# Optimization experiments

Measured on AMD Instinct MI355X. Metric: run time of the kernel, lower is better.

## Reference

```python
import jax, jax.numpy as jnp
import numpy as np

B, L, V = 128, 32, 10000
IC, WD, H = 2048, 512, 512  # image_code_dim, word_dim, hidden_size (num_layers=1)
D = WD + IC  # GRU input dim


def setup_inputs() -> dict:
    key = jax.random.key(0)
    ks = jax.random.split(key, 10)
    image_code = jax.random.normal(ks[0], (B, IC), dtype=jnp.float32)
    captions = jax.random.randint(ks[1], (B, L), 0, V)
    cap_lens = jax.random.randint(ks[2], (B,), 2, L + 1)
    cap_lens = cap_lens.at[0].set(L)  # pin max length -> static T = L-1
    # parameters (embed/fc match init_weights uniform(-0.1,0.1); GRU/init_state ~ small random)
    embed_w = jax.random.uniform(ks[3], (V, WD), minval=-0.1, maxval=0.1, dtype=jnp.float32)
    W_ih = jax.random.normal(ks[4], (3 * H, D), dtype=jnp.float32) * 0.02
    W_hh = jax.random.normal(ks[5], (3 * H, H), dtype=jnp.float32) * 0.02
    b_ih = jnp.zeros((3 * H,), dtype=jnp.float32)
    b_hh = jnp.zeros((3 * H,), dtype=jnp.float32)
    fc_w = jax.random.uniform(ks[6], (V, H), minval=-0.1, maxval=0.1, dtype=jnp.float32)
    fc_b = jnp.zeros((V,), dtype=jnp.float32)
    init_w = jax.random.normal(ks[7], (H, IC), dtype=jnp.float32) * 0.02  # num_layers*H x IC
    init_b = jnp.zeros((H,), dtype=jnp.float32)
    return {"image_code": image_code, "captions": captions, "cap_lens": cap_lens,
            "embed_w": embed_w, "W_ih": W_ih, "W_hh": W_hh, "b_ih": b_ih, "b_hh": b_hh,
            "fc_w": fc_w, "fc_b": fc_b, "init_w": init_w, "init_b": init_b}


def _gru_decode(image_code, captions_s, lengths, h0, embed_w, W_ih, W_hh, b_ih, b_hh, fc_w, fc_b):
    T = L - 1
    emb = embed_w[captions_s]                      # (B, L, WD)
    xs = jnp.concatenate([
        jnp.broadcast_to(image_code[None], (T, B, IC)),
        jnp.transpose(emb[:, :T, :], (1, 0, 2)),   # (T, B, WD)
    ], axis=-1)                                    # (T, B, D)

    def step(h, x_t):
        gi = x_t @ W_ih.T + b_ih                   # (B, 3H)
        gh = h @ W_hh.T + b_hh                     # (B, 3H)
        i_r, i_z, i_n = jnp.split(gi, 3, axis=-1)
        h_r, h_z, h_n = jnp.split(gh, 3, axis=-1)
        r = jax.nn.sigmoid(i_r + h_r)
        z = jax.nn.sigmoid(i_z + h_z)
        n = jnp.tanh(i_n + r * h_n)
        h_new = (1.0 - z) * n + z * h
        return h_new, h_new

    _, outs = jax.lax.scan(step, h0, xs)           # (T, B, H)
    preds = jnp.einsum('tbh,vh->tbv', outs, fc_w) + fc_b  # dropout is identity in eval
    mask = jnp.arange(T)[:, None] < lengths[None, :]      # (T, B): only active steps
    preds = jnp.where(mask[:, :, None], preds, 0.0)
    return jnp.transpose(preds, (1, 0, 2))         # (B, T, V)


def reference(image_code, captions, cap_lens, embed_w, W_ih, W_hh, b_ih, b_hh, fc_w, fc_b, init_w, init_b):
    order = jnp.argsort(-cap_lens)                 # descending sort like torch.sort(..., True)
    sorted_lens = cap_lens[order]
    captions_s = captions[order]
    image_code_s = image_code[order]
    h0 = image_code_s @ init_w.T + init_b          # (B, H) (num_layers = 1)
    lengths = sorted_lens - 1
    predictions = _gru_decode(image_code_s, captions_s, lengths, h0,
                              embed_w, W_ih, W_hh, b_ih, b_hh, fc_w, fc_b)
    return predictions, captions_s, lengths, order
```

## Files before the change

### kernel.cpp

```cpp
#include <hip/hip_runtime.h>
#include <math.h>

#define B_   128
#define L_   32
#define T_   31
#define V_   10000
#define IC_  2048
#define WD_  512
#define H_   512
#define D_   2560
#define G3_  1536
#define NPAD_ 10112
#define NPROD_ 64
#define NCONS_ 395
#define NTEAM_ 5

typedef short short8 __attribute__((ext_vector_type(8)));
typedef float f32x4  __attribute__((ext_vector_type(4)));
typedef unsigned short ushort_t;
typedef unsigned long long ull_t;

__device__ __forceinline__ unsigned short f2bf(float f) {
    unsigned int u = __builtin_bit_cast(unsigned int, f);
    unsigned int r = (u + 0x7FFFu + ((u >> 16) & 1u)) >> 16;
    return (unsigned short)r;
}
__device__ __forceinline__ float bf2f(unsigned short h) {
    unsigned int u = ((unsigned int)h) << 16;
    return __builtin_bit_cast(float, u);
}
__device__ __forceinline__ f32x4 mfma16(short8 a, short8 b, f32x4 c) {
    return __builtin_amdgcn_mfma_f32_16x16x32_bf16(a, b, c, 0, 0, 0);
}

#define WS_ORDER  0
#define WS_LEN    512
#define WS_TOK    1024
#define WS_BAR    16896
#define WS_GIIMG  16960
#define WS_WHH    803392
#define WS_GIFULL 2376256
#define WS_OUTS   14565952
#define WS_FCW    18760256

__global__ void k_prep(const int* __restrict__ captions,
                       const int* __restrict__ cap_lens,
                       int* __restrict__ order,
                       int* __restrict__ len_i,
                       int* __restrict__ tok,
                       int* __restrict__ bar,
                       float* __restrict__ out_tail) {
    __shared__ int s_len[B_];
    __shared__ int s_ord[B_];
    const int tid = threadIdx.x;
    if (tid == 0) *bar = 0;
    if (tid < B_) s_len[tid] = cap_lens[tid];
    __syncthreads();
    if (tid < B_) {
        const int myl = s_len[tid];
        int rank = 0;
        for (int k = 0; k < B_; ++k) {
            const int lk = s_len[k];
            if (lk > myl || (lk == myl && k < tid)) rank++;
        }
        s_ord[rank] = tid;
    }
    __syncthreads();
    if (tid < B_) {
        const int o = s_ord[tid];
        order[tid] = o;
        const int ln = s_len[o] - 1;
        len_i[tid] = ln;
        out_tail[B_ * L_ + tid]      = (float)ln;
        out_tail[B_ * L_ + B_ + tid] = (float)o;
    }
    __syncthreads();
    for (int i = tid; i < B_ * L_; i += blockDim.x) {
        const int b = i / L_, l = i % L_;
        const int c = captions[s_ord[b] * L_ + l];
        out_tail[i] = (float)c;
        if (l < T_) tok[l * B_ + b] = c;
    }
}

__global__ void k_cvt_fcw(const float* __restrict__ src, ushort_t* __restrict__ dst) {
    const int idx = blockIdx.x * 256 + threadIdx.x;
    const int row = idx >> 6;
    const int ch  = idx & 63;
    union { unsigned short u[8]; uint4 v; } r;
    if (row < V_) {
        const float* p = src + (size_t)row * 512 + ch * 8;
        const float4 x = *(const float4*)p;
        const float4 y = *(const float4*)(p + 4);
        r.u[0]=f2bf(x.x); r.u[1]=f2bf(x.y); r.u[2]=f2bf(x.z); r.u[3]=f2bf(x.w);
        r.u[4]=f2bf(y.x); r.u[5]=f2bf(y.y); r.u[6]=f2bf(y.z); r.u[7]=f2bf(y.w);
    } else {
        r.v = make_uint4(0, 0, 0, 0);
    }
    *(uint4*)&dst[(size_t)row * 512 + ch * 8] = r.v;
}

__global__ void k_cvt_whh(const float* __restrict__ whh, ushort_t* __restrict__ dst) {
    const int idx = blockIdx.x * 256 + threadIdx.x;
    const size_t o = (size_t)idx * 8;
    const int g = (int)(o / (48 * 512));
    const int rem = (int)(o % (48 * 512));
    const int j = rem >> 9;
    const int k = rem & 511;
    const int srow = (j >> 4) * 512 + g * 16 + (j & 15);
    const float* p = whh + (size_t)srow * 512 + k;
    const float4 x = *(const float4*)p;
    const float4 y = *(const float4*)(p + 4);
    union { unsigned short u[8]; uint4 v; } r;
    r.u[0]=f2bf(x.x); r.u[1]=f2bf(x.y); r.u[2]=f2bf(x.z); r.u[3]=f2bf(x.w);
    r.u[4]=f2bf(y.x); r.u[5]=f2bf(y.y); r.u[6]=f2bf(y.z); r.u[7]=f2bf(y.w);
    *(uint4*)&dst[o] = r.v;
}

template<bool F32>
__device__ __forceinline__ uint4 load_cvt(const void* src, size_t off) {
    if constexpr (!F32) {
        return *(const uint4*)((const unsigned short*)src + off);
    } else {
        const float* p = (const float*)src + off;
        const float4 x = *(const float4*)p;
        const float4 y = *(const float4*)(p + 4);
        union { unsigned short u[8]; uint4 v; } r;
        r.u[0]=f2bf(x.x); r.u[1]=f2bf(x.y); r.u[2]=f2bf(x.z); r.u[3]=f2bf(x.w);
        r.u[4]=f2bf(y.x); r.u[5]=f2bf(y.y); r.u[6]=f2bf(y.z); r.u[7]=f2bf(y.w);
        return r.v;
    }
}

struct EpiAdd2D {
    ushort_t* C; int ldc; const float* add; int addld; const float* bhh;
    __device__ void operator()(int m, int n, float v) const {
        const float extra = (n < 1024) ? bhh[n] : 0.f;
        C[(size_t)m * ldc + n] = f2bf(v + add[(size_t)(m & 127) * addld + n] + extra);
    }
};

template<bool AF32, bool BF32, class Epi>
__global__ __launch_bounds__(256) void gemm128(
    const void* __restrict__ A, int lda, const int* __restrict__ gidx,
    const void* __restrict__ Bm, int ldb, int K, Epi epi)
{
    __shared__ ushort_t As[128 * 32];
    __shared__ ushort_t Bs[128 * 32];
    const int tid = threadIdx.x;
    const int m0 = blockIdx.y * 128, n0 = blockIdx.x * 128;
    const int w = tid >> 6, lane = tid & 63, quad = lane >> 4, lr = lane & 15;
    const int srow = tid >> 2, ch = tid & 3;
    const int wm = (w & 1) * 64, wn = (w >> 1) * 64;

    const int ar0 = gidx ? gidx[m0 + srow]      : (m0 + srow);
    const int ar1 = gidx ? gidx[m0 + srow + 64] : (m0 + srow + 64);
    const int br0 = n0 + srow, br1 = n0 + srow + 64;

    f32x4 acc[4][4];
    const f32x4 z4 = {0.f, 0.f, 0.f, 0.f};
#pragma unroll
    for (int i = 0; i < 4; ++i)
#pragma unroll
        for (int j = 0; j < 4; ++j) acc[i][j] = z4;

    uint4 a0 = load_cvt<AF32>(A, (size_t)ar0 * lda + ch * 8);
    uint4 a1 = load_cvt<AF32>(A, (size_t)ar1 * lda + ch * 8);
    uint4 b0 = load_cvt<BF32>(Bm, (size_t)br0 * ldb + ch * 8);
    uint4 b1 = load_cvt<BF32>(Bm, (size_t)br1 * ldb + ch * 8);

    for (int k0 = 0; k0 < K; k0 += 32) {
        __syncthreads();
        *(uint4*)&As[(srow)      * 32 + ch * 8] = a0;
        *(uint4*)&As[(srow + 64) * 32 + ch * 8] = a1;
        *(uint4*)&Bs[(srow)      * 32 + ch * 8] = b0;
        *(uint4*)&Bs[(srow + 64) * 32 + ch * 8] = b1;
        __syncthreads();
        short8 af[4], bfr[4];
#pragma unroll
        for (int i = 0; i < 4; ++i) af[i]  = *(const short8*)&As[(wm + i * 16 + lr) * 32 + quad * 8];
#pragma unroll
        for (int j = 0; j < 4; ++j) bfr[j] = *(const short8*)&Bs[(wn + j * 16 + lr) * 32 + quad * 8];
        if (k0 + 32 < K) {
            a0 = load_cvt<AF32>(A, (size_t)ar0 * lda + k0 + 32 + ch * 8);
            a1 = load_cvt<AF32>(A, (size_t)ar1 * lda + k0 + 32 + ch * 8);
            b0 = load_cvt<BF32>(Bm, (size_t)br0 * ldb + k0 + 32 + ch * 8);
            b1 = load_cvt<BF32>(Bm, (size_t)br1 * ldb + k0 + 32 + ch * 8);
        }
#pragma unroll
        for (int i = 0; i < 4; ++i)
#pragma unroll
            for (int j = 0; j < 4; ++j) acc[i][j] = mfma16(af[i], bfr[j], acc[i][j]);
    }

#pragma unroll
    for (int i = 0; i < 4; ++i)
#pragma unroll
        for (int r = 0; r < 4; ++r) {
            const int m = m0 + wm + i * 16 + quad * 4 + r;
#pragma unroll
            for (int j = 0; j < 4; ++j) {
                const int n = n0 + wn + j * 16 + lr;
                epi(m, n, acc[i][j][r]);
            }
        }
}

__global__ __launch_bounds__(256) void k_pfx(
    const float* __restrict__ image_code,
    const int* __restrict__ order,
    const float* __restrict__ W_ih,
    const float* __restrict__ b_ih,
    const float* __restrict__ init_w,
    const float* __restrict__ init_b,
    float* __restrict__ gi_img,
    ushort_t* __restrict__ outs)
{
    __shared__ ushort_t As[128 * 32];
    __shared__ ushort_t Bs[128 * 32];
    const int tid = threadIdx.x;
    const int bx = blockIdx.x;
    const bool isH0 = bx >= 12;
    const float* Bm = isH0 ? init_w : W_ih;
    const int ldb = isH0 ? IC_ : D_;
    const int n0 = isH0 ? (bx - 12) * 128 : bx * 128;
    const float* bias = isH0 ? init_b : b_ih;

    const int w = tid >> 6, lane = tid & 63, quad = lane >> 4, lr = lane & 15;
    const int srow = tid >> 2, ch = tid & 3;
    const int wm = (w & 1) * 64, wn = (w >> 1) * 64;

    const int ar0 = order[srow];
    const int ar1 = order[srow + 64];
    const int br0 = n0 + srow, br1 = n0 + srow + 64;

    f32x4 acc[4][4];
    const f32x4 z4 = {0.f, 0.f, 0.f, 0.f};
#pragma unroll
    for (int i = 0; i < 4; ++i)
#pragma unroll
        for (int j = 0; j < 4; ++j) acc[i][j] = z4;

    uint4 a0 = load_cvt<true>(image_code, (size_t)ar0 * IC_ + ch * 8);
    uint4 a1 = load_cvt<true>(image_code, (size_t)ar1 * IC_ + ch * 8);
    uint4 b0 = load_cvt<true>(Bm, (size_t)br0 * ldb + ch * 8);
    uint4 b1 = load_cvt<true>(Bm, (size_t)br1 * ldb + ch * 8);

    for (int k0 = 0; k0 < IC_; k0 += 32) {
        __syncthreads();
        *(uint4*)&As[(srow)      * 32 + ch * 8] = a0;
        *(uint4*)&As[(srow + 64) * 32 + ch * 8] = a1;
        *(uint4*)&Bs[(srow)      * 32 + ch * 8] = b0;
        *(uint4*)&Bs[(srow + 64) * 32 + ch * 8] = b1;
        __syncthreads();
        short8 af[4], bfr[4];
#pragma unroll
        for (int i = 0; i < 4; ++i) af[i]  = *(const short8*)&As[(wm + i * 16 + lr) * 32 + quad * 8];
#pragma unroll
        for (int j = 0; j < 4; ++j) bfr[j] = *(const short8*)&Bs[(wn + j * 16 + lr) * 32 + quad * 8];
        if (k0 + 32 < IC_) {
            a0 = load_cvt<true>(image_code, (size_t)ar0 * IC_ + k0 + 32 + ch * 8);
            a1 = load_cvt<true>(image_code, (size_t)ar1 * IC_ + k0 + 32 + ch * 8);
            b0 = load_cvt<true>(Bm, (size_t)br0 * ldb + k0 + 32 + ch * 8);
            b1 = load_cvt<true>(Bm, (size_t)br1 * ldb + k0 + 32 + ch * 8);
        }
#pragma unroll
        for (int i = 0; i < 4; ++i)
#pragma unroll
            for (int j = 0; j < 4; ++j) acc[i][j] = mfma16(af[i], bfr[j], acc[i][j]);
    }

#pragma unroll
    for (int i = 0; i < 4; ++i)
#pragma unroll
        for (int r = 0; r < 4; ++r) {
            const int m = wm + i * 16 + quad * 4 + r;
#pragma unroll
            for (int j = 0; j < 4; ++j) {
                const int n = n0 + wn + j * 16 + lr;
                const float v = acc[i][j][r] + bias[n];
                if (isH0) outs[(size_t)m * H_ + n] = f2bf(v);
                else      gi_img[(size_t)m * G3_ + n] = v;
            }
        }
}

#define PBS_STR 520
__global__ __launch_bounds__(256, 2) void k_fused(
    const ushort_t* __restrict__ whh_bf,
    const ushort_t* __restrict__ gi_full,
    const float* __restrict__ b_hh,
    ushort_t* __restrict__ outs,
    const ushort_t* __restrict__ fcw_bf,
    const float* __restrict__ fc_b,
    const int* __restrict__ len_i,
    float* __restrict__ out,
    int* __restrict__ sync)
{
    __shared__ __align__(16) ushort_t sm[48 * PBS_STR];
    const int bid = blockIdx.x;
    const int tid = threadIdx.x;
    const int w = tid >> 6, lane = tid & 63, quad = lane >> 4, lr = lane & 15;

    if (bid < NPROD_) {
        __builtin_amdgcn_s_setprio(1);
        const int g = bid & 31;
        const int ih = bid >> 5;
        const bool leader = (bid == (ih << 5));
        ushort_t* Bs = sm;

        const ushort_t* wsrc = whh_bf + (size_t)g * 48 * 512;
        for (int i = tid; i < 48 * 64; i += 256) {
            const int row = i >> 6, c = i & 63;
            *(uint4*)&Bs[row * PBS_STR + c * 8] = *(const uint4*)&wsrc[row * 512 + c * 8];
        }
        const int cg = g * 16 + lr;
        const float bhn = b_hh[1024 + cg];
        __syncthreads();

        float hold_reg[4];
        {
            const ushort_t* h0p = outs + (size_t)ih * 64 * 512;
#pragma unroll
            for (int r = 0; r < 4; ++r)
                hold_reg[r] = bf2f(h0p[(size_t)(w * 16 + quad * 4 + r) * 512 + cg]);
        }
        ushort_t gi0[4], gi1[4], gi2[4];
#pragma unroll
        for (int r = 0; r < 4; ++r) {
            const int b = ih * 64 + w * 16 + quad * 4 + r;
            const ushort_t* p = gi_full + (size_t)b * G3_ + cg;
            gi0[r] = p[0]; gi1[r] = p[512]; gi2[r] = p[1024];
        }

        for (int step = 0; step < T_; ++step) {
            const ushort_t* hsrc = outs + (size_t)step * (128 * 512) + (size_t)ih * 64 * 512;

            uint4 hv[16];
            const ushort_t* hrow = hsrc + (size_t)(w * 16 + lr) * 512 + quad * 8;
#pragma unroll
            for (int kk = 0; kk < 16; ++kk)
                hv[kk] = *(const uint4*)(hrow + kk * 32);

            f32x4 acc[3];
#pragma unroll
            for (int j = 0; j < 3; ++j) acc[j] = (f32x4){0.f, 0.f, 0.f, 0.f};
#pragma unroll
            for (int kk = 0; kk < 16; ++kk) {
                union { uint4 v; short8 s; } cc; cc.v = hv[kk];
                const short8 af = cc.s;
#pragma unroll
                for (int j = 0; j < 3; ++j) {
                    const short8 bf = *(const short8*)&Bs[(j * 16 + lr) * PBS_STR + kk * 32 + quad * 8];
                    acc[j] = mfma16(af, bf, acc[j]);
                }
            }

            ushort_t* hdst = outs + (size_t)(step + 1) * (128 * 512);
#pragma unroll
            for (int r = 0; r < 4; ++r) {
                const int b = ih * 64 + w * 16 + quad * 4 + r;
                const float ir  = bf2f(gi0[r]);
                const float iz  = bf2f(gi1[r]);
                const float in_ = bf2f(gi2[r]);
                const float hr = acc[0][r];
                const float hz = acc[1][r];
                const float hn = acc[2][r] + bhn;
                const float rg = 1.f / (1.f + __expf(-(ir + hr)));
                const float zg = 1.f / (1.f + __expf(-(iz + hz)));
                const float nn = tanhf(in_ + rg * hn);
                const float hnew = (1.f - zg) * nn + zg * hold_reg[r];
                const unsigned int hb = (unsigned int)f2bf(hnew);
                hold_reg[r] = bf2f((unsigned short)hb);
                const unsigned int pv = (unsigned int)__shfl_xor((int)hb, 1);
                if ((lr & 1) == 0) {
                    const unsigned int word = hb | (pv << 16);
                    __hip_atomic_store((unsigned int*)&hdst[(size_t)b * 512 + cg], word,
                                       __ATOMIC_RELAXED, __HIP_MEMORY_SCOPE_AGENT);
                }
            }

            asm volatile("s_waitcnt vmcnt(0)" ::: "memory");
            __syncthreads();
            const int tgt = step + 1;
            if (tid == 0)
                __hip_atomic_store(&sync[bid * 8], tgt,
                                   __ATOMIC_RELAXED, __HIP_MEMORY_SCOPE_AGENT);

            ushort_t ng0[4], ng1[4], ng2[4];
            if (step + 1 < T_) {
                const size_t gb = (size_t)(step + 1) * 128 * G3_;
#pragma unroll
                for (int r = 0; r < 4; ++r) {
                    const int b = ih * 64 + w * 16 + quad * 4 + r;
                    const ushort_t* p = gi_full + gb + (size_t)b * G3_ + cg;
                    ng0[r] = p[0]; ng1[r] = p[512]; ng2[r] = p[1024];
                }
            }
            asm volatile("" ::: "memory");

            if (w == 0 && (step < T_ - 1 || leader)) {
                const int* pf = &sync[(ih * 32 + (lane & 31)) * 8];
                for (;;) {
                    const int v = __hip_atomic_load(pf, __ATOMIC_RELAXED, __HIP_MEMORY_SCOPE_AGENT);
                    if (__all(v >= tgt)) break;
                    __builtin_amdgcn_s_sleep(1);
                }
                if (leader && lane == 0) {
#pragma unroll
                    for (int k = 0; k < 8; ++k)
                        __hip_atomic_store(&sync[768 + k * 16 + ih], tgt,
                                           __ATOMIC_RELAXED, __HIP_MEMORY_SCOPE_AGENT);
                }
            }
            __syncthreads();
            asm volatile("" ::: "memory");

            if (step + 1 < T_) {
#pragma unroll
                for (int r = 0; r < 4; ++r) { gi0[r] = ng0[r]; gi1[r] = ng1[r]; gi2[r] = ng2[r]; }
            }
        }
    } else {
        const int cid = bid - NPROD_;
        const int nb = cid % 79;
        const int team = cid / 79;
        const int n0 = nb * 128;
        ushort_t* As = sm;
        ushort_t* Bs = sm + 4096;
        const int srow = tid >> 2, ch = tid & 3;
        const int wm = (w & 1) * 64, wn = (w >> 1) * 64;
        const ull_t* hready = (const ull_t*)&sync[768 + (cid & 7) * 16];

        float fcb[4];
#pragma unroll
        for (int j = 0; j < 4; ++j) {
            const int n = n0 + wn + j * 16 + lr;
            fcb[j] = (n < V_) ? fc_b[n] : 0.f;
        }

        for (int t = team; t < T_; t += NTEAM_) {
            if (tid == 0) {
                for (;;) {
                    const ull_t hv8 = __hip_atomic_load(hready, __ATOMIC_RELAXED, __HIP_MEMORY_SCOPE_AGENT);
                    const int l0 = (int)(unsigned int)(hv8 & 0xffffffffull);
                    const int l1 = (int)(unsigned int)(hv8 >> 32);
                    if (l0 > t && l1 > t) break;
                    __builtin_amdgcn_s_sleep(16);
                }
            }
            __syncthreads();

            const ushort_t* A = outs + (size_t)(t + 1) * (128 * 512);

            f32x4 acc[4][4];
            const f32x4 z4 = {0.f, 0.f, 0.f, 0.f};
#pragma unroll
            for (int i = 0; i < 4; ++i)
#pragma unroll
                for (int j = 0; j < 4; ++j) acc[i][j] = z4;

            uint4 a0 = *(const uint4*)&A[(size_t)srow * 512 + ch * 8];
            uint4 a1 = *(const uint4*)&A[(size_t)(srow + 64) * 512 + ch * 8];
            uint4 b0 = *(const uint4*)&fcw_bf[(size_t)(n0 + srow)      * 512 + ch * 8];
            uint4 b1 = *(const uint4*)&fcw_bf[(size_t)(n0 + srow + 64) * 512 + ch * 8];

            for (int k0 = 0; k0 < 512; k0 += 32) {
                __syncthreads();
                *(uint4*)&As[(srow)      * 32 + ch * 8] = a0;
                *(uint4*)&As[(srow + 64) * 32 + ch * 8] = a1;
                *(uint4*)&Bs[(srow)      * 32 + ch * 8] = b0;
                *(uint4*)&Bs[(srow + 64) * 32 + ch * 8] = b1;
                __syncthreads();
                short8 af[4], bfr[4];
#pragma unroll
                for (int i = 0; i < 4; ++i) af[i]  = *(const short8*)&As[(wm + i * 16 + lr) * 32 + quad * 8];
#pragma unroll
                for (int j = 0; j < 4; ++j) bfr[j] = *(const short8*)&Bs[(wn + j * 16 + lr) * 32 + quad * 8];
                if (k0 + 32 < 512) {
                    a0 = *(const uint4*)&A[(size_t)srow * 512 + k0 + 32 + ch * 8];
                    a1 = *(const uint4*)&A[(size_t)(srow + 64) * 512 + k0 + 32 + ch * 8];
                    b0 = *(const uint4*)&fcw_bf[(size_t)(n0 + srow)      * 512 + k0 + 32 + ch * 8];
                    b1 = *(const uint4*)&fcw_bf[(size_t)(n0 + srow + 64) * 512 + k0 + 32 + ch * 8];
                }
#pragma unroll
                for (int i = 0; i < 4; ++i)
#pragma unroll
                    for (int j = 0; j < 4; ++j) acc[i][j] = mfma16(af[i], bfr[j], acc[i][j]);
            }

#pragma unroll
            for (int i = 0; i < 4; ++i)
#pragma unroll
                for (int r = 0; r < 4; ++r) {
                    const int b = wm + i * 16 + quad * 4 + r;
                    const bool act = (t < len_i[b]);
                    const size_t base = (size_t)b * T_ * V_ + (size_t)t * V_;
#pragma unroll
                    for (int j = 0; j < 4; ++j) {
                        const int n = n0 + wn + j * 16 + lr;
                        if (n < V_) out[base + n] = act ? (acc[i][j][r] + fcb[j]) : 0.f;
                    }
                }
        }
    }
}

extern "C" void kernel_launch(void* const* d_in, const int* in_sizes, int n_in,
                              void* d_out, int out_size, void* d_ws, size_t ws_size,
                              hipStream_t stream) {
    const float* image_code = (const float*)d_in[0];
    const int*   captions   = (const int*)d_in[1];
    const int*   cap_lens   = (const int*)d_in[2];
    const float* embed_w    = (const float*)d_in[3];
    const float* W_ih       = (const float*)d_in[4];
    const float* W_hh       = (const float*)d_in[5];
    const float* b_ih       = (const float*)d_in[6];
    const float* b_hh       = (const float*)d_in[7];
    const float* fc_w       = (const float*)d_in[8];
    const float* fc_b       = (const float*)d_in[9];
    const float* init_w     = (const float*)d_in[10];
    const float* init_b     = (const float*)d_in[11];

    float* out = (float*)d_out;
    char* ws = (char*)d_ws;
    int*      order   = (int*)(ws + WS_ORDER);
    int*      len_i   = (int*)(ws + WS_LEN);
    int*      tok     = (int*)(ws + WS_TOK);
    int*      bar     = (int*)(ws + WS_BAR);
    float*    gi_img  = (float*)(ws + WS_GIIMG);
    ushort_t* whh_bf  = (ushort_t*)(ws + WS_WHH);
    ushort_t* gi_full = (ushort_t*)(ws + WS_GIFULL);
    ushort_t* outs_bf = (ushort_t*)(ws + WS_OUTS);
    ushort_t* fcw_bf  = (ushort_t*)(ws + WS_FCW);
    int*      sync    = (int*)(fcw_bf + ((size_t)NPAD_ - 4) * 512);

    hipLaunchKernelGGL(k_prep, dim3(1), dim3(128), 0, stream,
                       captions, cap_lens, order, len_i, tok, bar,
                       out + (size_t)B_ * T_ * V_);

    hipLaunchKernelGGL(k_cvt_fcw, dim3((NPAD_ * 64) / 256), dim3(256), 0, stream,
                       fc_w, fcw_bf);
    hipLaunchKernelGGL(k_cvt_whh, dim3((G3_ * H_ / 8) / 256), dim3(256), 0, stream,
                       W_hh, whh_bf);

    hipLaunchKernelGGL(k_pfx, dim3(16), dim3(256), 0, stream,
                       image_code, order, W_ih, b_ih, init_w, init_b,
                       gi_img, outs_bf);

    hipLaunchKernelGGL((gemm128<true, true, EpiAdd2D>), dim3(12, 31), dim3(256), 0, stream,
                       embed_w, WD_, tok, W_ih + IC_, D_, WD_,
                       EpiAdd2D{gi_full, G3_, gi_img, G3_, b_hh});

    hipLaunchKernelGGL(k_fused, dim3(NPROD_ + NCONS_), dim3(256), 0, stream,
                       whh_bf, gi_full, b_hh, outs_bf,
                       fcw_bf, fc_b, len_i, out, sync);
}
```

Before: 538.0 us.

## Merge setup kernels into one launch and shrink consumer grid with larger LDS tiles

Folds the prep, fc_w and W_hh bf16 conversion, and image-prefix GEMM kernels into a single k_setup launch. Each prefix block recomputes the sort locally so it no longer waits on a separate prep kernel. The fused decode kernel drops from 395 to 158 consumer blocks with 2 teams instead of 5, and its shared buffer grows to 43008 elements at one block per CU. This removes launch and serialization overhead but changes consumer parallelism and occupancy. The consumer body that depends on NCONS_/NTEAM_ is not shown.

```diff
diff --git a/kernel.cpp b/kernel.cpp
--- a/kernel.cpp
+++ b/kernel.cpp
@@ -12,8 +12,12 @@
 #define G3_  1536
 #define NPAD_ 10112
 #define NPROD_ 64
-#define NCONS_ 395
-#define NTEAM_ 5
+#define NCONS_ 158
+#define NTEAM_ 2
+#define SU_PFX0 1
+#define SU_FCW0 17
+#define SU_WHH0 (SU_FCW0 + 2528)
+#define SU_N    (SU_WHH0 + 384)
 
 typedef short short8 __attribute__((ext_vector_type(8)));
 typedef float f32x4  __attribute__((ext_vector_type(4)));
@@ -42,80 +46,6 @@
 #define WS_GIFULL 2376256
 #define WS_OUTS   14565952
 #define WS_FCW    18760256
-
-__global__ void k_prep(const int* __restrict__ captions,
-                       const int* __restrict__ cap_lens,
-                       int* __restrict__ order,
-                       int* __restrict__ len_i,
-                       int* __restrict__ tok,
-                       int* __restrict__ bar,
-                       float* __restrict__ out_tail) {
-    __shared__ int s_len[B_];
-    __shared__ int s_ord[B_];
-    const int tid = threadIdx.x;
-    if (tid == 0) *bar = 0;
-    if (tid < B_) s_len[tid] = cap_lens[tid];
-    __syncthreads();
-    if (tid < B_) {
-        const int myl = s_len[tid];
-        int rank = 0;
-        for (int k = 0; k < B_; ++k) {
-            const int lk = s_len[k];
-            if (lk > myl || (lk == myl && k < tid)) rank++;
-        }
-        s_ord[rank] = tid;
-    }
-    __syncthreads();
-    if (tid < B_) {
-        const int o = s_ord[tid];
-        order[tid] = o;
-        const int ln = s_len[o] - 1;
-        len_i[tid] = ln;
-        out_tail[B_ * L_ + tid]      = (float)ln;
-        out_tail[B_ * L_ + B_ + tid] = (float)o;
-    }
-    __syncthreads();
-    for (int i = tid; i < B_ * L_; i += blockDim.x) {
-        const int b = i / L_, l = i % L_;
-        const int c = captions[s_ord[b] * L_ + l];
-        out_tail[i] = (float)c;
-        if (l < T_) tok[l * B_ + b] = c;
-    }
-}
-
-__global__ void k_cvt_fcw(const float* __restrict__ src, ushort_t* __restrict__ dst) {
-    const int idx = blockIdx.x * 256 + threadIdx.x;
-    const int row = idx >> 6;
-    const int ch  = idx & 63;
-    union { unsigned short u[8]; uint4 v; } r;
-    if (row < V_) {
-        const float* p = src + (size_t)row * 512 + ch * 8;
-        const float4 x = *(const float4*)p;
-        const float4 y = *(const float4*)(p + 4);
-        r.u[0]=f2bf(x.x); r.u[1]=f2bf(x.y); r.u[2]=f2bf(x.z); r.u[3]=f2bf(x.w);
-        r.u[4]=f2bf(y.x); r.u[5]=f2bf(y.y); r.u[6]=f2bf(y.z); r.u[7]=f2bf(y.w);
-    } else {
-        r.v = make_uint4(0, 0, 0, 0);
-    }
-    *(uint4*)&dst[(size_t)row * 512 + ch * 8] = r.v;
-}
-
-__global__ void k_cvt_whh(const float* __restrict__ whh, ushort_t* __restrict__ dst) {
-    const int idx = blockIdx.x * 256 + threadIdx.x;
-    const size_t o = (size_t)idx * 8;
-    const int g = (int)(o / (48 * 512));
-    const int rem = (int)(o % (48 * 512));
-    const int j = rem >> 9;
-    const int k = rem & 511;
-    const int srow = (j >> 4) * 512 + g * 16 + (j & 15);
-    const float* p = whh + (size_t)srow * 512 + k;
-    const float4 x = *(const float4*)p;
-    const float4 y = *(const float4*)(p + 4);
-    union { unsigned short u[8]; uint4 v; } r;
-    r.u[0]=f2bf(x.x); r.u[1]=f2bf(x.y); r.u[2]=f2bf(x.z); r.u[3]=f2bf(x.w);
-    r.u[4]=f2bf(y.x); r.u[5]=f2bf(y.y); r.u[6]=f2bf(y.z); r.u[7]=f2bf(y.w);
-    *(uint4*)&dst[o] = r.v;
-}
 
 template<bool F32>
 __device__ __forceinline__ uint4 load_cvt(const void* src, size_t off) {
@@ -132,6 +62,167 @@
     }
 }
 
+__global__ __launch_bounds__(256) void k_setup(
+    const int* __restrict__ captions,
+    const int* __restrict__ cap_lens,
+    const float* __restrict__ fc_w,
+    const float* __restrict__ W_hh,
+    const float* __restrict__ image_code,
+    const float* __restrict__ W_ih,
+    const float* __restrict__ b_ih,
+    const float* __restrict__ init_w,
+    const float* __restrict__ init_b,
+    ushort_t* __restrict__ fcw_bf,
+    ushort_t* __restrict__ whh_bf,
+    float* __restrict__ gi_img,
+    ushort_t* __restrict__ outs,
+    int* __restrict__ order,
+    int* __restrict__ len_i,
+    int* __restrict__ tok,
+    int* __restrict__ bar,
+    float* __restrict__ out_tail)
+{
+    __shared__ __align__(16) ushort_t As[128 * 32];
+    __shared__ __align__(16) ushort_t Bs[128 * 32];
+    __shared__ int s_len[B_];
+    __shared__ int s_ord[B_];
+    const int bid = blockIdx.x;
+    const int tid = threadIdx.x;
+
+    if (bid >= SU_FCW0 && bid < SU_WHH0) {
+        const int idx = (bid - SU_FCW0) * 256 + tid;
+        const int row = idx >> 6;
+        const int ch  = idx & 63;
+        union { unsigned short u[8]; uint4 v; } r;
+        if (row < V_) {
+            const float* p = fc_w + (size_t)row * 512 + ch * 8;
+            const float4 x = *(const float4*)p;
+            const float4 y = *(const float4*)(p + 4);
+            r.u[0]=f2bf(x.x); r.u[1]=f2bf(x.y); r.u[2]=f2bf(x.z); r.u[3]=f2bf(x.w);
+            r.u[4]=f2bf(y.x); r.u[5]=f2bf(y.y); r.u[6]=f2bf(y.z); r.u[7]=f2bf(y.w);
+        } else {
+            r.v = make_uint4(0, 0, 0, 0);
+        }
+        *(uint4*)&fcw_bf[(size_t)row * 512 + ch * 8] = r.v;
+        return;
+    }
+    if (bid >= SU_WHH0) {
+        const int idx = (bid - SU_WHH0) * 256 + tid;
+        const size_t o = (size_t)idx * 8;
+        const int g = (int)(o / (48 * 512));
+        const int rem = (int)(o % (48 * 512));
+        const int j = rem >> 9;
+        const int k = rem & 511;
+        const int srow = (j >> 4) * 512 + g * 16 + (j & 15);
+        const float* p = W_hh + (size_t)srow * 512 + k;
+        const float4 x = *(const float4*)p;
+        const float4 y = *(const float4*)(p + 4);
+        union { unsigned short u[8]; uint4 v; } r;
+        r.u[0]=f2bf(x.x); r.u[1]=f2bf(x.y); r.u[2]=f2bf(x.z); r.u[3]=f2bf(x.w);
+        r.u[4]=f2bf(y.x); r.u[5]=f2bf(y.y); r.u[6]=f2bf(y.z); r.u[7]=f2bf(y.w);
+        *(uint4*)&whh_bf[o] = r.v;
+        return;
+    }
+
+    if (tid < B_) s_len[tid] = cap_lens[tid];
+    __syncthreads();
+    if (tid < B_) {
+        const int myl = s_len[tid];
+        int rank = 0;
+        for (int k = 0; k < B_; ++k) {
+            const int lk = s_len[k];
+            if (lk > myl || (lk == myl && k < tid)) rank++;
+        }
+        s_ord[rank] = tid;
+    }
+    __syncthreads();
+
+    if (bid == 0) {
+        if (tid == 0) *bar = 0;
+        if (tid < B_) {
+            const int o = s_ord[tid];
+            order[tid] = o;
+            const int ln = s_len[o] - 1;
+            len_i[tid] = ln;
+            out_tail[B_ * L_ + tid]      = (float)ln;
+            out_tail[B_ * L_ + B_ + tid] = (float)o;
+        }
+        __syncthreads();
+        for (int i = tid; i < B_ * L_; i += 256) {
+            const int b = i / L_, l = i % L_;
+            const int c = captions[s_ord[b] * L_ + l];
+            out_tail[i] = (float)c;
+            if (l < T_) tok[l * B_ + b] = c;
+        }
+        return;
+    }
+
+    const int px = bid - SU_PFX0;
+    const bool isH0 = px >= 12;
+    const float* Bm = isH0 ? init_w : W_ih;
+    const int ldb = isH0 ? IC_ : D_;
+    const int n0 = isH0 ? (px - 12) * 128 : px * 128;
+    const float* bias = isH0 ? init_b : b_ih;
+
+    const int w = tid >> 6, lane = tid & 63, quad = lane >> 4, lr = lane & 15;
+    const int srow = tid >> 2, ch = tid & 3;
+    const int wm = (w & 1) * 64, wn = (w >> 1) * 64;
+
+    const int ar0 = s_ord[srow];
+    const int ar1 = s_ord[srow + 64];
+    const int br0 = n0 + srow, br1 = n0 + srow + 64;
+
+    f32x4 acc[4][4];
+    const f32x4 z4 = {0.f, 0.f, 0.f, 0.f};
+#pragma unroll
+    for (int i = 0; i < 4; ++i)
+#pragma unroll
+        for (int j = 0; j < 4; ++j) acc[i][j] = z4;
+
+    uint4 a0 = load_cvt<true>(image_code, (size_t)ar0 * IC_ + ch * 8);
+    uint4 a1 = load_cvt<true>(image_code, (size_t)ar1 * IC_ + ch * 8);
+    uint4 b0 = load_cvt<true>(Bm, (size_t)br0 * ldb + ch * 8);
+    uint4 b1 = load_cvt<true>(Bm, (size_t)br1 * ldb + ch * 8);
+
+    for (int k0 = 0; k0 < IC_; k0 += 32) {
+        __syncthreads();
+        *(uint4*)&As[(srow)      * 32 + ch * 8] = a0;
+        *(uint4*)&As[(srow + 64) * 32 + ch * 8] = a1;
+        *(uint4*)&Bs[(srow)      * 32 + ch * 8] = b0;
+        *(uint4*)&Bs[(srow + 64) * 32 + ch * 8] = b1;
+        __syncthreads();
+        short8 af[4], bfr[4];
+#pragma unroll
+        for (int i = 0; i < 4; ++i) af[i]  = *(const short8*)&As[(wm + i * 16 + lr) * 32 + quad * 8];
+#pragma unroll
+        for (int j = 0; j < 4; ++j) bfr[j] = *(const short8*)&Bs[(wn + j * 16 + lr) * 32 + quad * 8];
+        if (k0 + 32 < IC_) {
+            a0 = load_cvt<true>(image_code, (size_t)ar0 * IC_ + k0 + 32 + ch * 8);
+            a1 = load_cvt<true>(image_code, (size_t)ar1 * IC_ + k0 + 32 + ch * 8);
+            b0 = load_cvt<true>(Bm, (size_t)br0 * ldb + k0 + 32 + ch * 8);
+            b1 = load_cvt<true>(Bm, (size_t)br1 * ldb + k0 + 32 + ch * 8);
+        }
+#pragma unroll
+        for (int i = 0; i < 4; ++i)
+#pragma unroll
+            for (int j = 0; j < 4; ++j) acc[i][j] = mfma16(af[i], bfr[j], acc[i][j]);
+    }
+
+#pragma unroll
+    for (int i = 0; i < 4; ++i)
+#pragma unroll
+        for (int r = 0; r < 4; ++r) {
+            const int m = wm + i * 16 + quad * 4 + r;
+#pragma unroll
+            for (int j = 0; j < 4; ++j) {
+                const int n = n0 + wn + j * 16 + lr;
+                const float v = acc[i][j][r] + bias[n];
+                if (isH0) outs[(size_t)m * H_ + n] = f2bf(v);
+                else      gi_img[(size_t)m * G3_ + n] = v;
+            }
+        }
+}
+
 struct EpiAdd2D {
     ushort_t* C; int ldc; const float* add; int addld; const float* bhh;
     __device__ void operator()(int m, int n, float v) const {
@@ -206,87 +297,8 @@
         }
 }
 
-__global__ __launch_bounds__(256) void k_pfx(
-    const float* __restrict__ image_code,
-    const int* __restrict__ order,
-    const float* __restrict__ W_ih,
-    const float* __restrict__ b_ih,
-    const float* __restrict__ init_w,
-    const float* __restrict__ init_b,
-    float* __restrict__ gi_img,
-    ushort_t* __restrict__ outs)
-{
-    __shared__ ushort_t As[128 * 32];
-    __shared__ ushort_t Bs[128 * 32];
-    const int tid = threadIdx.x;
-    const int bx = blockIdx.x;
-    const bool isH0 = bx >= 12;
-    const float* Bm = isH0 ? init_w : W_ih;
-    const int ldb = isH0 ? IC_ : D_;
-    const int n0 = isH0 ? (bx - 12) * 128 : bx * 128;
-    const float* bias = isH0 ? init_b : b_ih;
-
-    const int w = tid >> 6, lane = tid & 63, quad = lane >> 4, lr = lane & 15;
-    const int srow = tid >> 2, ch = tid & 3;
-    const int wm = (w & 1) * 64, wn = (w >> 1) * 64;
-
-    const int ar0 = order[srow];
-    const int ar1 = order[srow + 64];
-    const int br0 = n0 + srow, br1 = n0 + srow + 64;
-
-    f32x4 acc[4][4];
-    const f32x4 z4 = {0.f, 0.f, 0.f, 0.f};
-#pragma unroll
-    for (int i = 0; i < 4; ++i)
-#pragma unroll
-        for (int j = 0; j < 4; ++j) acc[i][j] = z4;
-
-    uint4 a0 = load_cvt<true>(image_code, (size_t)ar0 * IC_ + ch * 8);
-    uint4 a1 = load_cvt<true>(image_code, (size_t)ar1 * IC_ + ch * 8);
-    uint4 b0 = load_cvt<true>(Bm, (size_t)br0 * ldb + ch * 8);
-    uint4 b1 = load_cvt<true>(Bm, (size_t)br1 * ldb + ch * 8);
-
-    for (int k0 = 0; k0 < IC_; k0 += 32) {
-        __syncthreads();
-        *(uint4*)&As[(srow)      * 32 + ch * 8] = a0;
-        *(uint4*)&As[(srow + 64) * 32 + ch * 8] = a1;
-        *(uint4*)&Bs[(srow)      * 32 + ch * 8] = b0;
-        *(uint4*)&Bs[(srow + 64) * 32 + ch * 8] = b1;
-        __syncthreads();
-        short8 af[4], bfr[4];
-#pragma unroll
-        for (int i = 0; i < 4; ++i) af[i]  = *(const short8*)&As[(wm + i * 16 + lr) * 32 + quad * 8];
-#pragma unroll
-        for (int j = 0; j < 4; ++j) bfr[j] = *(const short8*)&Bs[(wn + j * 16 + lr) * 32 + quad * 8];
-        if (k0 + 32 < IC_) {
-            a0 = load_cvt<true>(image_code, (size_t)ar0 * IC_ + k0 + 32 + ch * 8);
-            a1 = load_cvt<true>(image_code, (size_t)ar1 * IC_ + k0 + 32 + ch * 8);
-            b0 = load_cvt<true>(Bm, (size_t)br0 * ldb + k0 + 32 + ch * 8);
-            b1 = load_cvt<true>(Bm, (size_t)br1 * ldb + k0 + 32 + ch * 8);
-        }
-#pragma unroll
-        for (int i = 0; i < 4; ++i)
-#pragma unroll
-            for (int j = 0; j < 4; ++j) acc[i][j] = mfma16(af[i], bfr[j], acc[i][j]);
-    }
-
-#pragma unroll
-    for (int i = 0; i < 4; ++i)
-#pragma unroll
-        for (int r = 0; r < 4; ++r) {
-            const int m = wm + i * 16 + quad * 4 + r;
-#pragma unroll
-            for (int j = 0; j < 4; ++j) {
-                const int n = n0 + wn + j * 16 + lr;
-                const float v = acc[i][j][r] + bias[n];
-                if (isH0) outs[(size_t)m * H_ + n] = f2bf(v);
-                else      gi_img[(size_t)m * G3_ + n] = v;
-            }
-        }
-}
-
 #define PBS_STR 520
-__global__ __launch_bounds__(256, 2) void k_fused(
+__global__ __launch_bounds__(256, 1) void k_fused(
     const ushort_t* __restrict__ whh_bf,
     const ushort_t* __restrict__ gi_full,
     const float* __restrict__ b_hh,
@@ -297,7 +309,7 @@
     float* __restrict__ out,
     int* __restrict__ sync)
 {
-    __shared__ __align__(16) ushort_t sm[48 * PBS_STR];
+    __shared__ __align__(16) ushort_t sm[43008];
     const int bid = blockIdx.x;
     const int tid = threadIdx.x;
     const int w = tid >> 6, lane = tid & 63, quad = lane >> 4, lr = lane & 15;
@@ -535,18 +547,12 @@
     ushort_t* fcw_bf  = (ushort_t*)(ws + WS_FCW);
     int*      sync    = (int*)(fcw_bf + ((size_t)NPAD_ - 4) * 512);
 
-    hipLaunchKernelGGL(k_prep, dim3(1), dim3(128), 0, stream,
-                       captions, cap_lens, order, len_i, tok, bar,
+    hipLaunchKernelGGL(k_setup, dim3(SU_N), dim3(256), 0, stream,
+                       captions, cap_lens, fc_w, W_hh,
+                       image_code, W_ih, b_ih, init_w, init_b,
+                       fcw_bf, whh_bf, gi_img, outs_bf,
+                       order, len_i, tok, bar,
                        out + (size_t)B_ * T_ * V_);
-
-    hipLaunchKernelGGL(k_cvt_fcw, dim3((NPAD_ * 64) / 256), dim3(256), 0, stream,
-                       fc_w, fcw_bf);
-    hipLaunchKernelGGL(k_cvt_whh, dim3((G3_ * H_ / 8) / 256), dim3(256), 0, stream,
-                       W_hh, whh_bf);
-
-    hipLaunchKernelGGL(k_pfx, dim3(16), dim3(256), 0, stream,
-                       image_code, order, W_ih, b_ih, init_w, init_b,
-                       gi_img, outs_bf);
 
     hipLaunchKernelGGL((gemm128<true, true, EpiAdd2D>), dim3(12, 31), dim3(256), 0, stream,
                        embed_w, WD_, tok, W_ih + IC_, D_, WD_,
```

New measurement: 498.2 us. 1.08x faster.
